# Performance work log

Measured on AMD Instinct MI355X. Metric: run time of the kernel, lower is better.

## Reference

```python
import jax, jax.numpy as jnp
import numpy as np

N_NODES = 370
N_EEG = 64
HID = 64
L = 8
KS = 2
EMB = 16
KTOP = N_NODES // 10  # 37, as in the torch code


def _gcn_norm_dense(A):
    # A[dst, src] dense adjacency. torch_geometric GCNConv gcn_norm:
    # add self-loop weight 1.0 only for nodes lacking one, then D^-1/2 A D^-1/2.
    d0 = jnp.diagonal(A)
    A = A + jnp.diag(jnp.where(d0 > 0, 0.0, 1.0))
    deg = A.sum(axis=1)  # weighted in-degree at dst (incl. self loops)
    dinv = jnp.where(deg > 0, jax.lax.rsqrt(deg), 0.0)
    return dinv[:, None] * A * dinv[None, :]


def _adaptive_adj(emb_src, emb_tgt):
    # softmax(relu(S T^T)) row-wise, keep top-k per row (softmax vals are all >0)
    adj = jax.nn.softmax(jax.nn.relu(emb_src @ emb_tgt.T), axis=-1)
    vals, idx = jax.lax.top_k(adj, KTOP)
    sp = jnp.zeros_like(adj).at[jnp.arange(adj.shape[0])[:, None], idx].set(vals)
    return _gcn_norm_dense(sp)


def _causal_conv(h, w, b, dilation):
    # h: (BN, H, T), w: (H_out, H_in, K); left-pad by (K-1)*dilation => causal
    pad = (w.shape[-1] - 1) * dilation
    out = jax.lax.conv_general_dilated(
        h, w, window_strides=(1,), padding=[(pad, 0)],
        rhs_dilation=(dilation,), dimension_numbers=("NCH", "OIH", "NCH"))
    return out + b[None, :, None]


def _layernorm(x, g, b, eps=1e-5):
    m = x.mean(-1, keepdims=True)
    v = ((x - m) ** 2).mean(-1, keepdims=True)
    return (x - m) * jax.lax.rsqrt(v + eps) * g + b


def _gelu(x):
    return jax.nn.gelu(x, approximate=False)


def setup_inputs() -> dict:
    key = jax.random.key(0)
    ks = iter(jax.random.split(key, 64))
    B, T, E = 8, 64, 7400

    x = jax.random.normal(next(ks), (B, T, N_NODES, HID), jnp.float32)
    src = jax.random.randint(next(ks), (E,), 0, N_NODES, jnp.int32)
    off = jax.random.randint(next(ks), (E,), 1, N_NODES, jnp.int32)
    edge_index = jnp.stack([src, (src + off) % N_NODES])  # self-loop free
    edge_weight = jax.random.uniform(next(ks), (E,), jnp.float32)

    def rn(shape, scale):
        return jax.random.normal(next(ks), shape, jnp.float32) * scale

    s = 1.0 / np.sqrt(HID)
    inp = {
        "x": x, "edge_index": edge_index, "edge_weight": edge_weight,
        "in_W": rn((HID, HID), s), "in_b": rn((HID,), 0.01),
        "gcnf_W": rn((L, HID, HID), s), "gcnf_b": rn((L, HID), 0.01),
        "emb_src": rn((L, N_NODES, EMB), 1.0),  # torch.randn init
        "emb_tgt": rn((L, N_NODES, EMB), 1.0),
        "gcna_W": rn((L, HID, HID), s), "gcna_b": rn((L, HID), 0.01),
        "filt_W": rn((L, HID, HID, KS), s), "filt_b": rn((L, HID), 0.01),
        "gate_W": rn((L, HID, HID, KS), s), "gate_b": rn((L, HID), 0.01),
        "res_W": rn((L, HID, HID), s), "res_b": rn((L, HID), 0.01),
        "skip_W": rn((L, HID, HID), s), "skip_b": rn((L, HID), 0.01),
        "ln_g": jnp.ones((L, HID), jnp.float32), "ln_b": jnp.zeros((L, HID), jnp.float32),
        "end1_W": rn((HID, HID), s), "end1_b": rn((HID,), 0.01),
        "end2_W": rn((HID, HID), s), "end2_b": rn((HID,), 0.01),
        "eeg1_W": rn((N_NODES * HID, 256), 1.0 / np.sqrt(N_NODES * HID)), "eeg1_b": rn((256,), 0.01),
        "eeg2_W": rn((256, N_EEG), 1.0 / 16.0), "eeg2_b": rn((N_EEG,), 0.01),
    }
    return inp


def reference(x, edge_index, edge_weight, in_W, in_b, gcnf_W, gcnf_b,
              emb_src, emb_tgt, gcna_W, gcna_b, filt_W, filt_b, gate_W, gate_b,
              res_W, res_b, skip_W, skip_b, ln_g, ln_b,
              end1_W, end1_b, end2_W, end2_b, eeg1_W, eeg1_b, eeg2_W, eeg2_b):
    B, T, N, H = x.shape
    x = x @ in_W + in_b  # input_proj

    # Fixed (DTI prior) adjacency: same for every layer, build & normalize once.
    A = jnp.zeros((N, N), x.dtype).at[edge_index[1], edge_index[0]].add(edge_weight)
    A = _gcn_norm_dense(A)

    skip_sum = jnp.zeros_like(x)
    for i in range(L):  # fixed small layer count
        dil = 2 ** (i % 4)
        xf = x.reshape(B * T, N, H)
        h_fixed = jnp.einsum("mn,bnh->bmh", A, xf @ gcnf_W[i]) + gcnf_b[i]
        Aa = _adaptive_adj(emb_src[i], emb_tgt[i])
        h_adapt = jnp.einsum("mn,bnh->bmh", Aa, xf @ gcna_W[i]) + gcna_b[i]
        h = (h_fixed + h_adapt).reshape(B, T, N, H)
        h = h.transpose(0, 2, 3, 1).reshape(B * N, H, T)
        h = jnp.tanh(_causal_conv(h, filt_W[i], filt_b[i], dil)) * \
            jax.nn.sigmoid(_causal_conv(h, gate_W[i], gate_b[i], dil))
        # 1x1 convs over channel dim (dropout is identity in eval)
        skip = (jnp.einsum("oi,nit->not", skip_W[i], h) + skip_b[i][None, :, None])
        res = (jnp.einsum("oi,nit->not", res_W[i], h) + res_b[i][None, :, None])
        skip = skip.reshape(B, N, H, T).transpose(0, 3, 1, 2)
        res = res.reshape(B, N, H, T).transpose(0, 3, 1, 2)
        x = _layernorm(res + x, ln_g[i], ln_b[i])
        skip_sum = skip_sum + skip

    h = _gelu(skip_sum) @ end1_W + end1_b
    h = _gelu(h) @ end2_W + end2_b
    h = h.reshape(B, T, N * H)  # GraphToEEG
    h = _gelu(h @ eeg1_W + eeg1_b) @ eeg2_W + eeg2_b
    return h
```

## Files before the change

kernel.cpp:

```cpp
#include <hip/hip_runtime.h>
#include <hip/hip_bf16.h>
#include <math.h>

typedef __attribute__((ext_vector_type(8))) short bf16x8;
typedef __attribute__((ext_vector_type(4))) float f32x4;
typedef unsigned short u16;
typedef unsigned int u32;
typedef unsigned long long u64;

#define NN 370
#define HH 64
#define LL 8
#define TT 64
#define BTOT 512
#define RR (BTOT*NN)
#define KTOPK 37
#define SPLITK 37

__device__ inline u16 f2bf(float f){
  __hip_bfloat16 h = __float2bfloat16(f);
  return __builtin_bit_cast(u16, h);
}
__device__ inline float bf2f(short s){
  u32 v = ((u32)(u16)s) << 16;
  return __builtin_bit_cast(float, v);
}
__device__ inline float gelu_f(float x){ return 0.5f * x * (1.0f + erff(x * 0.70710678118654752440f)); }

__device__ inline void sts16(char* lds, int row, int kb, int stride, bf16x8 v){
  *reinterpret_cast<bf16x8*>(lds + row*stride + (kb ^ ((row&7)<<4))) = v;
}
__device__ inline bf16x8 lds16(const char* lds, int row, int kb, int stride){
  return *reinterpret_cast<const bf16x8*>(lds + row*stride + (kb ^ ((row&7)<<4)));
}
__device__ inline bf16x8 gldB(const char* Bt, int c, int kb, int stride){
  return *reinterpret_cast<const bf16x8*>(Bt + c*stride + (kb ^ ((c&7)<<4)));
}
__device__ inline void copyB(char* dst, const u16* src, int bytes, int tid, int nthr){
  for(int o = tid*16; o < bytes; o += nthr*16)
    *reinterpret_cast<bf16x8*>(dst + o) =
      *reinterpret_cast<const bf16x8*>(reinterpret_cast<const char*>(src) + o);
}

template<int NT, int KT>
__device__ inline void mma_core(const char* sA, const char* sB, int strideA, int strideB,
                                f32x4* acc, int ln, int mt){
#pragma unroll
  for(int nt=0; nt<NT; ++nt) acc[nt] = f32x4{0.f,0.f,0.f,0.f};
#pragma unroll
  for(int kt=0; kt<KT; ++kt){
    int kb = kt*64 + ((ln>>4)<<4);
    bf16x8 a = lds16(sA, mt*16 + (ln&15), kb, strideA);
#pragma unroll
    for(int nt=0; nt<NT; ++nt){
      bf16x8 b = lds16(sB, nt*16 + (ln&15), kb, strideB);
      acc[nt] = __builtin_amdgcn_mfma_f32_16x16x32_bf16(a, b, acc[nt], 0, 0, 0);
    }
  }
}

__global__ void kzero(float* __restrict__ p, size_t n){
  for(size_t i = (size_t)blockIdx.x*256 + threadIdx.x; i < n; i += (size_t)gridDim.x*256) p[i] = 0.f;
}

__global__ void kbuildA(const int* __restrict__ ei, const float* __restrict__ ew, float* __restrict__ Araw, int E){
  int e = blockIdx.x*256 + threadIdx.x;
  if(e < E){
    int src = ei[e], dst = ei[E + e];
    atomicAdd(&Araw[dst*NN + src], ew[e]);
  }
}

__global__ __launch_bounds__(384) void knormF(float* __restrict__ Araw, float* __restrict__ dinvF){
  int i = threadIdx.x;
  if(i < NN){
    float d0 = Araw[i*NN+i];
    if(d0 == 0.f) Araw[i*NN+i] = 1.f;
    float s = 0.f;
    for(int j=0;j<NN;++j) s += Araw[i*NN+j];
    dinvF[i] = rsqrtf(s);
  }
}

__global__ __launch_bounds__(512) void kadapt(const float* __restrict__ esrc, const float* __restrict__ etgt,
                                              float* __restrict__ ArawA, float* __restrict__ dinvA){
  __shared__ float tgT[16][372];
  __shared__ float red[8];
  __shared__ u64 keys[512];
  __shared__ int diagflag;
  int i = blockIdx.x, l = blockIdx.y, tid = threadIdx.x;
  const float* Et = etgt + (size_t)l*NN*16;
  for(int idx = tid; idx < NN*16; idx += 512)
    tgT[idx & 15][idx >> 4] = Et[idx];
  float sr[16];
  const float* Es = esrc + ((size_t)l*NN + i)*16;
#pragma unroll
  for(int k=0;k<16;k++) sr[k] = Es[k];
  if(tid == 0) diagflag = 0;
  __syncthreads();
  bool act = tid < NN;
  float s = 0.f;
  if(act){
    float d = 0.f;
#pragma unroll
    for(int k=0;k<16;k++) d += sr[k]*tgT[k][tid];
    s = fmaxf(d, 0.f);
  }
  float v = act ? s : -1.f;
#pragma unroll
  for(int o=1;o<64;o<<=1) v = fmaxf(v, __shfl_xor(v,o,64));
  if((tid&63)==0) red[tid>>6] = v;
  __syncthreads();
  float mx = red[0];
#pragma unroll
  for(int q=1;q<8;q++) mx = fmaxf(mx, red[q]);
  __syncthreads();
  float e = act ? expf(s - mx) : 0.f;
  float t = e;
#pragma unroll
  for(int o=1;o<64;o<<=1) t += __shfl_xor(t,o,64);
  if((tid&63)==0) red[tid>>6] = t;
  __syncthreads();
  float sum = 0.f;
#pragma unroll
  for(int q=0;q<8;q++) sum += red[q];
  float p = e / sum;
  u32 fb = __builtin_bit_cast(u32, p);
  keys[tid] = act ? ((((u64)fb)<<32) | (u64)(0xFFFFFFFFu - (u32)tid)) : 0ULL;
  __syncthreads();
  for(int k2=2; k2<=512; k2<<=1){
    for(int j=k2>>1; j>0; j>>=1){
      int ixj = tid ^ j;
      if(ixj > tid){
        u64 a = keys[tid], b = keys[ixj];
        bool dirUp = ((tid & k2) == 0);
        if(dirUp ? (a < b) : (a > b)){ keys[tid] = b; keys[ixj] = a; }
      }
      __syncthreads();
    }
  }
  float myval = 0.f; int myidx = -1;
  if(tid < KTOPK){
    u64 kk = keys[tid];
    myidx = (int)(0xFFFFFFFFu - (u32)kk);
    myval = __builtin_bit_cast(float, (u32)(kk>>32));
    if(myidx == i) diagflag = 1;
  }
  __syncthreads();
  float dsum = (tid < KTOPK) ? myval : 0.f;
  if(tid < 64){
#pragma unroll
    for(int o=1;o<64;o<<=1) dsum += __shfl_xor(dsum,o,64);
    if(tid == 0) dinvA[l*NN + i] = rsqrtf(dsum + (diagflag ? 0.f : 1.f));
  }
  if(tid < KTOPK) ArawA[((size_t)l*NN + i)*NN + myidx] = myval;
  if(tid == 0 && !diagflag) ArawA[((size_t)l*NN + i)*NN + i] = 1.f;
}

__global__ void kacat(const float* __restrict__ Araw, const float* __restrict__ ArawA,
                      const float* __restrict__ dinvF, const float* __restrict__ dinvA,
                      u16* __restrict__ Acat){
  int idx = blockIdx.x*256 + threadIdx.x;
  if(idx >= LL*384*768) return;
  int k = idx % 768; int m = (idx / 768) % 384; int l = idx / (768*384);
  float v = 0.f;
  if(m < NN){
    if(k < 384){
      if(k < NN) v = dinvF[m]*Araw[m*NN+k]*dinvF[k];
    } else {
      int n = k - 384;
      if(n < NN) v = dinvA[l*NN+m]*ArawA[((size_t)l*NN+m)*NN+n]*dinvA[l*NN+n];
    }
  }
  Acat[idx] = f2bf(v);
}

__global__ void kbt_small(const float* __restrict__ inW, const float* __restrict__ e1W, const float* __restrict__ e2W,
                          u16* __restrict__ BtIN, u16* __restrict__ BtE1, u16* __restrict__ BtE2){
  const float* W = blockIdx.x==0 ? inW : (blockIdx.x==1 ? e1W : e2W);
  u16* Bt = blockIdx.x==0 ? BtIN : (blockIdx.x==1 ? BtE1 : BtE2);
  for(int idx = threadIdx.x; idx < 4096; idx += 256){
    int c = idx >> 6, k = idx & 63;
    *(u16*)((char*)Bt + c*128 + ((k*2) ^ ((c&7)<<4))) = f2bf(W[k*64 + c]);
  }
}

__global__ void kbt_layer(const float* __restrict__ gcnfW, const float* __restrict__ gcnaW,
                          const float* __restrict__ filtW, const float* __restrict__ gateW,
                          const float* __restrict__ skipW, const float* __restrict__ resW,
                          u16* __restrict__ BtUV, u16* __restrict__ BtCV, u16* __restrict__ BtSR){
  int l = blockIdx.x, which = blockIdx.y;
  if(which == 0){
    u16* Bt = BtUV + (size_t)l*128*64;
    for(int idx=threadIdx.x; idx<8192; idx+=256){
      int c = idx>>6, k = idx&63;
      float v = (c<64) ? gcnfW[(size_t)l*4096 + k*64 + c] : gcnaW[(size_t)l*4096 + k*64 + (c-64)];
      *(u16*)((char*)Bt + c*128 + ((k*2) ^ ((c&7)<<4))) = f2bf(v);
    }
  } else if(which == 1){
    u16* Bt = BtCV + (size_t)l*128*128;
    for(int idx=threadIdx.x; idx<16384; idx+=256){
      int c = idx>>7, k = idx&127;
      const float* W = (c<64) ? filtW : gateW;
      int o = c & 63, ii = k & 63, tap = (k<64) ? 1 : 0;
      float v = W[(size_t)l*8192 + o*128 + ii*2 + tap];
      *(u16*)((char*)Bt + c*256 + ((k*2) ^ ((c&7)<<4))) = f2bf(v);
    }
  } else {
    u16* Bt = BtSR + (size_t)l*128*64;
    for(int idx=threadIdx.x; idx<8192; idx+=256){
      int c = idx>>6, k = idx&63;
      float v = (c<64) ? skipW[(size_t)l*4096 + c*64 + k] : resW[(size_t)l*4096 + (c-64)*64 + k];
      *(u16*)((char*)Bt + c*128 + ((k*2) ^ ((c&7)<<4))) = f2bf(v);
    }
  }
}

__global__ void ktrans(const float* __restrict__ W, u16* __restrict__ Wt){
  __shared__ float tile[64][65];
  int kb = blockIdx.x*64, cb = blockIdx.y*64;
  for(int idx = threadIdx.x; idx < 4096; idx += 256){
    int kk = idx>>6, cc = idx&63;
    tile[kk][cc] = W[(size_t)(kb+kk)*256 + cb+cc];
  }
  __syncthreads();
  for(int idx = threadIdx.x; idx < 4096; idx += 256){
    int cc = idx>>6, kk = idx&63;
    Wt[(size_t)(cb+cc)*23680 + kb+kk] = f2bf(tile[kk][cc]);
  }
}

__global__ __launch_bounds__(256) void krowmm_in(const float* __restrict__ X, const u16* __restrict__ Bt,
                                                 const float* __restrict__ bias,
                                                 u16* __restrict__ xbf){
  int tid = threadIdx.x;
  int w = tid>>6, ln = tid&63, lr = ln&15, hi = ln>>4;
  int kboff = hi<<4;
  size_t r = (size_t)blockIdx.x*64 + w*16 + lr;
  f32x4 acc[4];
#pragma unroll
  for(int i=0;i<4;i++) acc[i] = f32x4{0.f,0.f,0.f,0.f};
  const char* BI = (const char*)Bt;
#pragma unroll
  for(int kt=0; kt<2; ++kt){
    const float* xr = X + r*64 + kt*32 + hi*8;
    float4 pa = ((const float4*)xr)[0], pb = ((const float4*)xr)[1];
    bf16x8 a;
    a[0]=(short)f2bf(pa.x); a[1]=(short)f2bf(pa.y); a[2]=(short)f2bf(pa.z); a[3]=(short)f2bf(pa.w);
    a[4]=(short)f2bf(pb.x); a[5]=(short)f2bf(pb.y); a[6]=(short)f2bf(pb.z); a[7]=(short)f2bf(pb.w);
#pragma unroll
    for(int nt=0; nt<4; ++nt){
      bf16x8 b = gldB(BI, nt*16 + lr, kt*64 + kboff, 128);
      acc[nt] = __builtin_amdgcn_mfma_f32_16x16x32_bf16(a, b, acc[nt], 0, 0, 0);
    }
  }
  size_t r0 = (size_t)blockIdx.x*64;
#pragma unroll
  for(int nt=0; nt<4; ++nt){
    int c = nt*16 + lr;
    float bv = bias[c];
#pragma unroll
    for(int rr=0;rr<4;++rr){
      int row = w*16 + hi*4 + rr;
      xbf[(r0+row)*64 + c] = f2bf(acc[nt][rr] + bv);
    }
  }
}

__global__ __launch_bounds__(1024) void kgcn(const u16* __restrict__ xbf, const u16* __restrict__ BtUV,
                                             const u16* __restrict__ Acat,
                                             const float* __restrict__ bfb, const float* __restrict__ bab,
                                             u16* __restrict__ t2){
  __shared__ char uvt[2*16384];
  int bt2 = blockIdx.x, tid = threadIdx.x;
  int w = tid>>6, ln = tid&63, lr = ln&15, hi = ln>>4;
  int kboff = hi<<4;
  int q = w>>3, wq = w&7;
  int bt = bt2*2 + q;
  const char* xb = (const char*)(xbf + (size_t)bt*NN*64);
  char* uq = uvt + q*16384;
  f32x4 acc[12];
#pragma unroll
  for(int j=0;j<12;j++) acc[j] = f32x4{0.f,0.f,0.f,0.f};
#pragma unroll
  for(int sp=0; sp<6; ++sp){
    int p = sp/3, third = sp - p*3;
    int nl = third*128 + wq*16 + lr;
    bf16x8 a0, a1;
    if(nl < NN){
      a0 = *reinterpret_cast<const bf16x8*>(xb + (size_t)nl*128 + kboff);
      a1 = *reinterpret_cast<const bf16x8*>(xb + (size_t)nl*128 + 64 + kboff);
    } else {
      bf16x8 z = {0,0,0,0,0,0,0,0}; a0 = z; a1 = z;
    }
    f32x4 uv[4];
#pragma unroll
    for(int nt=0;nt<4;++nt) uv[nt] = f32x4{0.f,0.f,0.f,0.f};
#pragma unroll
    for(int nt=0;nt<4;++nt){
      int c = p*64 + nt*16 + lr;
      bf16x8 b0 = gldB((const char*)BtUV, c, kboff, 128);
      bf16x8 b1 = gldB((const char*)BtUV, c, 64 + kboff, 128);
      uv[nt] = __builtin_amdgcn_mfma_f32_16x16x32_bf16(a0, b0, uv[nt], 0,0,0);
      uv[nt] = __builtin_amdgcn_mfma_f32_16x16x32_bf16(a1, b1, uv[nt], 0,0,0);
    }
    __syncthreads();
    int ndl = wq*16 + hi*4;
#pragma unroll
    for(int nt=0;nt<4;++nt){
      int cl = nt*16 + lr;
      u64 pk = (u64)((u32)f2bf(uv[nt][0]) | ((u32)f2bf(uv[nt][1])<<16))
             | ((u64)((u32)f2bf(uv[nt][2]) | ((u32)f2bf(uv[nt][3])<<16)) << 32);
      *(u64*)(uq + cl*256 + ((ndl*2) ^ ((cl&7)<<4))) = pk;
    }
    __syncthreads();
    const char* abase = (const char*)Acat + p*768 + third*256 + kboff;
#pragma unroll
    for(int kt=0; kt<4; ++kt){
      bf16x8 a_0 = *reinterpret_cast<const bf16x8*>(abase + (size_t)((wq*3+0)*16 + lr)*1536 + kt*64);
      bf16x8 a_1 = *reinterpret_cast<const bf16x8*>(abase + (size_t)((wq*3+1)*16 + lr)*1536 + kt*64);
      bf16x8 a_2 = *reinterpret_cast<const bf16x8*>(abase + (size_t)((wq*3+2)*16 + lr)*1536 + kt*64);
      bf16x8 b0 = lds16(uq, 0*16 + lr, kt*64 + kboff, 256);
      bf16x8 b1 = lds16(uq, 1*16 + lr, kt*64 + kboff, 256);
      bf16x8 b2 = lds16(uq, 2*16 + lr, kt*64 + kboff, 256);
      bf16x8 b3 = lds16(uq, 3*16 + lr, kt*64 + kboff, 256);
      acc[0]  = __builtin_amdgcn_mfma_f32_16x16x32_bf16(a_0, b0, acc[0],  0,0,0);
      acc[1]  = __builtin_amdgcn_mfma_f32_16x16x32_bf16(a_0, b1, acc[1],  0,0,0);
      acc[2]  = __builtin_amdgcn_mfma_f32_16x16x32_bf16(a_0, b2, acc[2],  0,0,0);
      acc[3]  = __builtin_amdgcn_mfma_f32_16x16x32_bf16(a_0, b3, acc[3],  0,0,0);
      acc[4]  = __builtin_amdgcn_mfma_f32_16x16x32_bf16(a_1, b0, acc[4],  0,0,0);
      acc[5]  = __builtin_amdgcn_mfma_f32_16x16x32_bf16(a_1, b1, acc[5],  0,0,0);
      acc[6]  = __builtin_amdgcn_mfma_f32_16x16x32_bf16(a_1, b2, acc[6],  0,0,0);
      acc[7]  = __builtin_amdgcn_mfma_f32_16x16x32_bf16(a_1, b3, acc[7],  0,0,0);
      acc[8]  = __builtin_amdgcn_mfma_f32_16x16x32_bf16(a_2, b0, acc[8],  0,0,0);
      acc[9]  = __builtin_amdgcn_mfma_f32_16x16x32_bf16(a_2, b1, acc[9],  0,0,0);
      acc[10] = __builtin_amdgcn_mfma_f32_16x16x32_bf16(a_2, b2, acc[10], 0,0,0);
      acc[11] = __builtin_amdgcn_mfma_f32_16x16x32_bf16(a_2, b3, acc[11], 0,0,0);
    }
  }
#pragma unroll
  for(int mi=0; mi<3; ++mi){
    int mt = wq*3 + mi;
    int mbase = mt*16 + hi*4;
#pragma unroll
    for(int nt=0; nt<4; ++nt){
      int col = nt*16 + lr;
      float bias = bfb[col] + bab[col];
#pragma unroll
      for(int r=0;r<4;++r){
        int m = mbase + r;
        if(m < NN) t2[((size_t)bt*NN + m)*64 + col] = f2bf(acc[mi*4+nt][r] + bias);
      }
    }
  }
}

__global__ __launch_bounds__(256) void kcsr(const u16* __restrict__ t2, const u16* __restrict__ BtC,
                                            const u16* __restrict__ BtS,
                                            const float* __restrict__ fb, const float* __restrict__ gb,
                                            const float* __restrict__ sb, const float* __restrict__ rb,
                                            const float* __restrict__ lng, const float* __restrict__ lnb,
                                            u16* __restrict__ skip,
                                            u16* __restrict__ xbf, int dil, int first, int douv){
  __shared__ char sA[32768];
  int blk = blockIdx.x, tid = threadIdx.x;
  int w = tid>>6, ln = tid&63, lr = ln&15, hi = ln>>4;
  int kboff = hi<<4;
  int r0 = blk*64;
  int r = r0 + w*16 + lr;
  int t = (r / NN) & (TT-1);
  const char* cur = (const char*)t2 + (size_t)r*128;
  const char* prv = cur - (size_t)dil*NN*128;
  bf16x8 a0 = *reinterpret_cast<const bf16x8*>(cur + kboff);
  bf16x8 a1 = *reinterpret_cast<const bf16x8*>(cur + 64 + kboff);
  bf16x8 a2, a3;
  if(t >= dil){
    a2 = *reinterpret_cast<const bf16x8*>(prv + kboff);
    a3 = *reinterpret_cast<const bf16x8*>(prv + 64 + kboff);
  } else {
    bf16x8 z = {0,0,0,0,0,0,0,0}; a2 = z; a3 = z;
  }
  const char* BC = (const char*)BtC;
  f32x4 acc[8];
#pragma unroll
  for(int i=0;i<8;i++) acc[i] = f32x4{0.f,0.f,0.f,0.f};
  bf16x8 afr[4] = {a0, a1, a2, a3};
#pragma unroll
  for(int kt=0; kt<4; ++kt){
    bf16x8 bfr[8];
#pragma unroll
    for(int nt=0; nt<8; ++nt)
      bfr[nt] = gldB(BC, nt*16 + lr, kt*64 + kboff, 256);
#pragma unroll
    for(int nt=0; nt<8; ++nt)
      acc[nt] = __builtin_amdgcn_mfma_f32_16x16x32_bf16(afr[kt], bfr[nt], acc[nt], 0, 0, 0);
  }
  u16 qv[4][4];
#pragma unroll
  for(int nt=0; nt<4; ++nt){
    int o = nt*16 + lr;
    float fbv = fb[o], gbv = gb[o];
#pragma unroll
    for(int rr=0;rr<4;++rr){
      float fv = acc[nt][rr] + fbv;
      float gv = acc[nt+4][rr] + gbv;
      float ef = __expf(-2.f*fv);
      float th = (1.f - ef) / (1.f + ef);
      float sg = 1.f / (1.f + __expf(-gv));
      qv[nt][rr] = f2bf(th * sg);
    }
  }
#pragma unroll
  for(int nt=0; nt<4; ++nt){
    int col = nt*16 + lr;
#pragma unroll
    for(int rr=0;rr<4;++rr){
      int row = w*16 + hi*4 + rr;
      *(u16*)(sA + row*128 + ((col*2) ^ ((row&7)<<4))) = qv[nt][rr];
    }
  }
  __syncthreads();
  const char* BS = (const char*)BtS;
  f32x4 as[8];
#pragma unroll
  for(int i=0;i<8;i++) as[i] = f32x4{0.f,0.f,0.f,0.f};
#pragma unroll
  for(int kt=0; kt<2; ++kt){
    bf16x8 a = lds16(sA, w*16 + lr, kt*64 + kboff, 128);
    bf16x8 bfr[8];
#pragma unroll
    for(int nt=0; nt<8; ++nt)
      bfr[nt] = gldB(BS, nt*16 + lr, kt*64 + kboff, 128);
#pragma unroll
    for(int nt=0; nt<8; ++nt)
      as[nt] = __builtin_amdgcn_mfma_f32_16x16x32_bf16(a, bfr[nt], as[nt], 0, 0, 0);
  }
  __syncthreads();
#pragma unroll
  for(int nt=0; nt<4; ++nt){
    int c = nt*16 + lr;
#pragma unroll
    for(int rr=0;rr<4;++rr){
      int row = w*16 + hi*4 + rr;
      *(float*)(sA + row*512 + (((c)*4)      ^ ((row&7)<<4))) = as[nt][rr];
      *(float*)(sA + row*512 + (((64+c)*4)   ^ ((row&7)<<4))) = as[4+nt][rr];
    }
  }
  __syncthreads();
  int row = tid >> 2, seg = tid & 3;
  int c0 = seg * 16;
  float sk[16], re[16];
#pragma unroll
  for(int j=0;j<4;++j){
    f32x4 vs = *reinterpret_cast<const f32x4*>(sA + row*512 + (((c0 + j*4)*4)      ^ ((row&7)<<4)));
    f32x4 vr = *reinterpret_cast<const f32x4*>(sA + row*512 + (((64 + c0 + j*4)*4) ^ ((row&7)<<4)));
#pragma unroll
    for(int i=0;i<4;++i){ sk[j*4+i] = vs[i]; re[j*4+i] = vr[i]; }
  }
  size_t gr = (size_t)(r0 + row)*64 + c0;
  bf16x8 xv0 = *reinterpret_cast<const bf16x8*>(xbf + gr);
  bf16x8 xv1 = *reinterpret_cast<const bf16x8*>(xbf + gr + 8);
  float y[16]; float s1 = 0.f, s2 = 0.f;
#pragma unroll
  for(int i=0;i<16;++i){
    float xo = bf2f(i < 8 ? xv0[i] : xv1[i-8]);
    float vv = re[i] + rb[c0+i] + xo;
    y[i] = vv; s1 += vv; s2 += vv*vv;
  }
  s1 += __shfl_xor(s1, 1, 64); s1 += __shfl_xor(s1, 2, 64);
  s2 += __shfl_xor(s2, 1, 64); s2 += __shfl_xor(s2, 2, 64);
  float m = s1 * (1.f/64.f);
  float var = s2 * (1.f/64.f) - m*m;
  float rstd = rsqrtf(var + 1e-5f);
  if(douv){
    bf16x8 o0, o1;
#pragma unroll
    for(int i=0;i<16;++i){
      float xo = (y[i] - m) * rstd * lng[c0+i] + lnb[c0+i];
      if(i < 8) o0[i] = (short)f2bf(xo); else o1[i-8] = (short)f2bf(xo);
    }
    *reinterpret_cast<bf16x8*>(xbf + gr) = o0;
    *reinterpret_cast<bf16x8*>(xbf + gr + 8) = o1;
  }
  bf16x8 so0, so1;
  if(first){
#pragma unroll
    for(int i=0;i<16;++i){
      float sv = sk[i] + sb[c0+i];
      if(i < 8) so0[i] = (short)f2bf(sv); else so1[i-8] = (short)f2bf(sv);
    }
  } else {
    bf16x8 sp0 = *reinterpret_cast<const bf16x8*>(skip + gr);
    bf16x8 sp1 = *reinterpret_cast<const bf16x8*>(skip + gr + 8);
#pragma unroll
    for(int i=0;i<16;++i){
      float old = bf2f(i < 8 ? sp0[i] : sp1[i-8]);
      float sv = old + sk[i] + sb[c0+i];
      if(i < 8) so0[i] = (short)f2bf(sv); else so1[i-8] = (short)f2bf(sv);
    }
  }
  *reinterpret_cast<bf16x8*>(skip + gr) = so0;
  *reinterpret_cast<bf16x8*>(skip + gr + 8) = so1;
}

__global__ __launch_bounds__(256) void kend2(const u16* __restrict__ skip, const u16* __restrict__ Bt1,
                                             const u16* __restrict__ Bt2, const float* __restrict__ b1,
                                             const float* __restrict__ b2, u16* __restrict__ h2){
  __shared__ char sA[8192];
  int tid = threadIdx.x;
  int w = tid>>6, ln = tid&63, lr = ln&15, hi = ln>>4;
  int kboff = hi<<4;
  size_t r = (size_t)blockIdx.x*64 + w*16 + lr;
  const char* B1 = (const char*)Bt1;
  const char* B2 = (const char*)Bt2;
  f32x4 acc[4];
#pragma unroll
  for(int i=0;i<4;i++) acc[i] = f32x4{0.f,0.f,0.f,0.f};
#pragma unroll
  for(int kt=0; kt<2; ++kt){
    bf16x8 a = *reinterpret_cast<const bf16x8*>((const char*)skip + r*128 + kt*64 + kboff);
#pragma unroll
    for(int i=0;i<8;i++) a[i] = (short)f2bf(gelu_f(bf2f(a[i])));
#pragma unroll
    for(int nt=0; nt<4; ++nt){
      bf16x8 b = gldB(B1, nt*16 + lr, kt*64 + kboff, 128);
      acc[nt] = __builtin_amdgcn_mfma_f32_16x16x32_bf16(a, b, acc[nt], 0, 0, 0);
    }
  }
  u16 xq[4][4];
#pragma unroll
  for(int nt=0; nt<4; ++nt){
    int c = nt*16 + lr;
    float bv = b1[c];
#pragma unroll
    for(int rr=0;rr<4;++rr) xq[nt][rr] = f2bf(gelu_f(acc[nt][rr] + bv));
  }
#pragma unroll
  for(int nt=0; nt<4; ++nt){
    int col = nt*16 + lr;
#pragma unroll
    for(int rr=0;rr<4;++rr){
      int row = w*16 + hi*4 + rr;
      *(u16*)(sA + row*128 + ((col*2) ^ ((row&7)<<4))) = xq[nt][rr];
    }
  }
  __syncthreads();
  f32x4 a2[4];
#pragma unroll
  for(int i=0;i<4;i++) a2[i] = f32x4{0.f,0.f,0.f,0.f};
#pragma unroll
  for(int kt=0; kt<2; ++kt){
    bf16x8 a = lds16(sA, w*16 + lr, kt*64 + kboff, 128);
#pragma unroll
    for(int nt=0; nt<4; ++nt){
      bf16x8 b = gldB(B2, nt*16 + lr, kt*64 + kboff, 128);
      a2[nt] = __builtin_amdgcn_mfma_f32_16x16x32_bf16(a, b, a2[nt], 0, 0, 0);
    }
  }
  size_t rbase = (size_t)blockIdx.x*64 + w*16 + hi*4;
#pragma unroll
  for(int nt=0; nt<4; ++nt){
    int c = nt*16 + lr;
    float bv = b2[c];
#pragma unroll
    for(int rr=0;rr<4;++rr) h2[(rbase+rr)*64 + c] = f2bf(a2[nt][rr] + bv);
  }
}

__global__ __launch_bounds__(512) void keeg1(const u16* __restrict__ h2, const u16* __restrict__ WtE,
                                             float* __restrict__ part){
  __shared__ char sA[64*128];
  __shared__ char sB[256*128];
  int rowg = blockIdx.x, sp = blockIdx.y;
  int tid = threadIdx.x, w = tid>>6, ln = tid&63;
  f32x4 acc[8];
#pragma unroll
  for(int i=0;i<8;i++) acc[i] = f32x4{0.f,0.f,0.f,0.f};
  int mt = w & 3, ntb = (w>>2)*8;
  for(int ks=0; ks<20; ++ks){
    int k0 = (sp*20 + ks)*32;
    __syncthreads();
    for(int s = tid; s < 256; s += 512){
      int row = s>>2, kc = s&3;
      bf16x8 v = *reinterpret_cast<const bf16x8*>(h2 + (size_t)(rowg*64+row)*23680 + k0 + kc*8);
      sts16(sA, row, kc*16, 128, v);
    }
    for(int s = tid; s < 1024; s += 512){
      int row = s>>2, kc = s&3;
      bf16x8 v = *reinterpret_cast<const bf16x8*>(WtE + (size_t)row*23680 + k0 + kc*8);
      sts16(sB, row, kc*16, 128, v);
    }
    __syncthreads();
    bf16x8 a = lds16(sA, mt*16 + (ln&15), ((ln>>4)<<4), 128);
#pragma unroll
    for(int j=0;j<8;++j){
      bf16x8 b = lds16(sB, (ntb+j)*16 + (ln&15), ((ln>>4)<<4), 128);
      acc[j] = __builtin_amdgcn_mfma_f32_16x16x32_bf16(a, b, acc[j], 0, 0, 0);
    }
  }
  float* dst = part + ((size_t)sp*512 + rowg*64)*256;
#pragma unroll
  for(int j=0;j<8;++j){
    int c = (ntb+j)*16 + (ln&15);
#pragma unroll
    for(int r=0;r<4;++r){
      int row = mt*16 + ((ln>>4)<<2) + r;
      dst[(size_t)row*256 + c] = acc[j][r];
    }
  }
}

__global__ __launch_bounds__(256) void keeg2(const float* __restrict__ part, const float* __restrict__ b1,
                                             const float* __restrict__ W2, const float* __restrict__ b2,
                                             float* __restrict__ out){
  __shared__ float u[256];
  __shared__ float pr[4][64];
  int bt = blockIdx.x, tid = threadIdx.x;
  float sacc = 0.f;
  for(int sp2=0; sp2<SPLITK; ++sp2) sacc += part[((size_t)sp2*512 + bt)*256 + tid];
  u[tid] = gelu_f(sacc + b1[tid]);
  __syncthreads();
  int w = tid>>6, ln = tid&63;
  float acc = 0.f;
  for(int c = w*64; c < (w+1)*64; ++c) acc += u[c] * W2[c*64 + ln];
  pr[w][ln] = acc;
  __syncthreads();
  if(tid < 64)
    out[(size_t)bt*64 + tid] = pr[0][tid]+pr[1][tid]+pr[2][tid]+pr[3][tid] + b2[tid];
}

extern "C" void kernel_launch(void* const* d_in, const int* in_sizes, int n_in,
                              void* d_out, int out_size, void* d_ws, size_t ws_size,
                              hipStream_t stream){
  const float* x_in  = (const float*)d_in[0];
  const int*   ei    = (const int*)d_in[1];
  const float* ew    = (const float*)d_in[2];
  const float* in_W  = (const float*)d_in[3];
  const float* in_b  = (const float*)d_in[4];
  const float* gcnfW = (const float*)d_in[5];
  const float* gcnfb = (const float*)d_in[6];
  const float* esrc  = (const float*)d_in[7];
  const float* etgt  = (const float*)d_in[8];
  const float* gcnaW = (const float*)d_in[9];
  const float* gcnab = (const float*)d_in[10];
  const float* filtW = (const float*)d_in[11];
  const float* filtb = (const float*)d_in[12];
  const float* gateW = (const float*)d_in[13];
  const float* gateb = (const float*)d_in[14];
  const float* resW  = (const float*)d_in[15];
  const float* resb  = (const float*)d_in[16];
  const float* skipW = (const float*)d_in[17];
  const float* skipb = (const float*)d_in[18];
  const float* lng   = (const float*)d_in[19];
  const float* lnb   = (const float*)d_in[20];
  const float* e1W   = (const float*)d_in[21];
  const float* e1b   = (const float*)d_in[22];
  const float* e2W   = (const float*)d_in[23];
  const float* e2b   = (const float*)d_in[24];
  const float* eg1W  = (const float*)d_in[25];
  const float* eg1b  = (const float*)d_in[26];
  const float* eg2W  = (const float*)d_in[27];
  const float* eg2b  = (const float*)d_in[28];
  int E = in_sizes[2];

  char* p = (char*)d_ws;
  auto carve = [&](size_t bytes)->char*{ char* r = p; p += (bytes + 255) & ~(size_t)255; return r; };
  u16*   xbf   = (u16*)  carve((size_t)RR*64*2);
  u16*   skip  = (u16*)  carve((size_t)RR*64*2);
  u16*   t2    = (u16*)  carve((size_t)RR*64*2);
  u16*   h2    = (u16*)  carve((size_t)RR*64*2);
  float* Araw9 = (float*)carve((size_t)9*NN*NN*4);
  float* Araw  = Araw9;
  float* ArawA = Araw9 + (size_t)NN*NN;
  float* dinvF = (float*)carve(NN*4);
  float* dinvA = (float*)carve(LL*NN*4);
  u16*   Acat  = (u16*)  carve((size_t)LL*384*768*2);
  u16*   BtUV  = (u16*)  carve((size_t)LL*128*64*2);
  u16*   BtCV  = (u16*)  carve((size_t)LL*128*128*2);
  u16*   BtSR  = (u16*)  carve((size_t)LL*128*64*2);
  u16*   BtIN  = (u16*)  carve(64*64*2);
  u16*   BtE1  = (u16*)  carve(64*64*2);
  u16*   BtE2  = (u16*)  carve(64*64*2);
  u16*   WtE   = (u16*)  carve((size_t)256*23680*2);
  float* part  = (float*)carve((size_t)SPLITK*512*256*4);

  kzero<<<1024, 256, 0, stream>>>(Araw9, (size_t)9*NN*NN);
  kbuildA<<<(E+255)/256, 256, 0, stream>>>(ei, ew, Araw, E);
  knormF<<<1, 384, 0, stream>>>(Araw, dinvF);
  kadapt<<<dim3(NN, LL), 512, 0, stream>>>(esrc, etgt, ArawA, dinvA);
  kacat<<<(LL*384*768 + 255)/256, 256, 0, stream>>>(Araw, ArawA, dinvF, dinvA, Acat);
  kbt_small<<<3, 256, 0, stream>>>(in_W, e1W, e2W, BtIN, BtE1, BtE2);
  kbt_layer<<<dim3(LL, 3), 256, 0, stream>>>(gcnfW, gcnaW, filtW, gateW, skipW, resW, BtUV, BtCV, BtSR);
  ktrans<<<dim3(370, 4), 256, 0, stream>>>(eg1W, WtE);

  krowmm_in<<<RR/64, 256, 0, stream>>>(x_in, BtIN, in_b, xbf);

  for(int l=0; l<LL; ++l){
    int dil = 1 << (l & 3);
    kgcn<<<BTOT/2, 1024, 0, stream>>>(xbf, BtUV + (size_t)l*8192, Acat + (size_t)l*384*768,
                                      gcnfb + l*64, gcnab + l*64, t2);
    int douv = (l < LL-1) ? 1 : 0;
    kcsr<<<RR/64, 256, 0, stream>>>(t2, BtCV + (size_t)l*16384, BtSR + (size_t)l*8192,
                                    filtb + l*64, gateb + l*64, skipb + l*64, resb + l*64,
                                    lng + l*64, lnb + l*64, skip, xbf, dil, l==0 ? 1 : 0, douv);
  }

  kend2<<<RR/64, 256, 0, stream>>>(skip, BtE1, BtE2, e1b, e2b, h2);
  keeg1<<<dim3(8, SPLITK), 512, 0, stream>>>(h2, WtE, part);
  keeg2<<<BTOT, 256, 0, stream>>>(part, eg1b, eg2W, eg2b, (float*)d_out);
}
```

Baseline: 1.019 ms.

## Double-buffer UV tiles in GCN kernel, one timestep per 512-thread block

The GCN kernel now processes one batch-time slice per 512-thread block instead of two slices per 1024-thread block, and reuses the freed shared memory as a double buffer for the UV tile. The next UV projection is computed while the adjacency MFMA for the current tile runs, which removes one of the two barriers per stage and overlaps the global loads with compute. In exchange it holds more registers for the prefetched UV values, which may lower occupancy, and it launches twice as many blocks.

```diff
diff --git a/kernel.cpp b/kernel.cpp
--- a/kernel.cpp
+++ b/kernel.cpp
@@ -267,25 +267,23 @@
   }
 }
 
-__global__ __launch_bounds__(1024) void kgcn(const u16* __restrict__ xbf, const u16* __restrict__ BtUV,
-                                             const u16* __restrict__ Acat,
-                                             const float* __restrict__ bfb, const float* __restrict__ bab,
-                                             u16* __restrict__ t2){
+__global__ __launch_bounds__(512) void kgcn(const u16* __restrict__ xbf, const u16* __restrict__ BtUV,
+                                            const u16* __restrict__ Acat,
+                                            const float* __restrict__ bfb, const float* __restrict__ bab,
+                                            u16* __restrict__ t2){
   __shared__ char uvt[2*16384];
-  int bt2 = blockIdx.x, tid = threadIdx.x;
+  int bt = blockIdx.x, tid = threadIdx.x;
   int w = tid>>6, ln = tid&63, lr = ln&15, hi = ln>>4;
   int kboff = hi<<4;
-  int q = w>>3, wq = w&7;
-  int bt = bt2*2 + q;
   const char* xb = (const char*)(xbf + (size_t)bt*NN*64);
-  char* uq = uvt + q*16384;
+  const char* BU = (const char*)BtUV;
   f32x4 acc[12];
 #pragma unroll
   for(int j=0;j<12;j++) acc[j] = f32x4{0.f,0.f,0.f,0.f};
-#pragma unroll
-  for(int sp=0; sp<6; ++sp){
+
+  auto UVC = [&](int sp, f32x4* uv){
     int p = sp/3, third = sp - p*3;
-    int nl = third*128 + wq*16 + lr;
+    int nl = third*128 + w*16 + lr;
     bf16x8 a0, a1;
     if(nl < NN){
       a0 = *reinterpret_cast<const bf16x8*>(xb + (size_t)nl*128 + kboff);
@@ -293,19 +291,24 @@
     } else {
       bf16x8 z = {0,0,0,0,0,0,0,0}; a0 = z; a1 = z;
     }
-    f32x4 uv[4];
 #pragma unroll
     for(int nt=0;nt<4;++nt) uv[nt] = f32x4{0.f,0.f,0.f,0.f};
 #pragma unroll
     for(int nt=0;nt<4;++nt){
       int c = p*64 + nt*16 + lr;
-      bf16x8 b0 = gldB((const char*)BtUV, c, kboff, 128);
-      bf16x8 b1 = gldB((const char*)BtUV, c, 64 + kboff, 128);
+      bf16x8 b0 = gldB(BU, c, kboff, 128);
+      bf16x8 b1 = gldB(BU, c, 64 + kboff, 128);
       uv[nt] = __builtin_amdgcn_mfma_f32_16x16x32_bf16(a0, b0, uv[nt], 0,0,0);
       uv[nt] = __builtin_amdgcn_mfma_f32_16x16x32_bf16(a1, b1, uv[nt], 0,0,0);
     }
-    __syncthreads();
-    int ndl = wq*16 + hi*4;
+  };
+
+  f32x4 uv[4];
+  UVC(0, uv);
+#pragma unroll
+  for(int sp=0; sp<6; ++sp){
+    char* uq = uvt + (sp&1)*16384;
+    int ndl = w*16 + hi*4;
 #pragma unroll
     for(int nt=0;nt<4;++nt){
       int cl = nt*16 + lr;
@@ -314,12 +317,15 @@
       *(u64*)(uq + cl*256 + ((ndl*2) ^ ((cl&7)<<4))) = pk;
     }
     __syncthreads();
+    f32x4 uvn[4];
+    if(sp < 5) UVC(sp+1, uvn);
+    int p = sp/3, third = sp - p*3;
     const char* abase = (const char*)Acat + p*768 + third*256 + kboff;
 #pragma unroll
     for(int kt=0; kt<4; ++kt){
-      bf16x8 a_0 = *reinterpret_cast<const bf16x8*>(abase + (size_t)((wq*3+0)*16 + lr)*1536 + kt*64);
-      bf16x8 a_1 = *reinterpret_cast<const bf16x8*>(abase + (size_t)((wq*3+1)*16 + lr)*1536 + kt*64);
-      bf16x8 a_2 = *reinterpret_cast<const bf16x8*>(abase + (size_t)((wq*3+2)*16 + lr)*1536 + kt*64);
+      bf16x8 a_0 = *reinterpret_cast<const bf16x8*>(abase + (size_t)((w*3+0)*16 + lr)*1536 + kt*64);
+      bf16x8 a_1 = *reinterpret_cast<const bf16x8*>(abase + (size_t)((w*3+1)*16 + lr)*1536 + kt*64);
+      bf16x8 a_2 = *reinterpret_cast<const bf16x8*>(abase + (size_t)((w*3+2)*16 + lr)*1536 + kt*64);
       bf16x8 b0 = lds16(uq, 0*16 + lr, kt*64 + kboff, 256);
       bf16x8 b1 = lds16(uq, 1*16 + lr, kt*64 + kboff, 256);
       bf16x8 b2 = lds16(uq, 2*16 + lr, kt*64 + kboff, 256);
@@ -337,10 +343,14 @@
       acc[10] = __builtin_amdgcn_mfma_f32_16x16x32_bf16(a_2, b2, acc[10], 0,0,0);
       acc[11] = __builtin_amdgcn_mfma_f32_16x16x32_bf16(a_2, b3, acc[11], 0,0,0);
     }
+    if(sp < 5){
+#pragma unroll
+      for(int nt=0;nt<4;++nt) uv[nt] = uvn[nt];
+    }
   }
 #pragma unroll
   for(int mi=0; mi<3; ++mi){
-    int mt = wq*3 + mi;
+    int mt = w*3 + mi;
     int mbase = mt*16 + hi*4;
 #pragma unroll
     for(int nt=0; nt<4; ++nt){
@@ -697,8 +707,8 @@
 
   for(int l=0; l<LL; ++l){
     int dil = 1 << (l & 3);
-    kgcn<<<BTOT/2, 1024, 0, stream>>>(xbf, BtUV + (size_t)l*8192, Acat + (size_t)l*384*768,
-                                      gcnfb + l*64, gcnab + l*64, t2);
+    kgcn<<<BTOT, 512, 0, stream>>>(xbf, BtUV + (size_t)l*8192, Acat + (size_t)l*384*768,
+                                   gcnfb + l*64, gcnab + l*64, t2);
     int douv = (l < LL-1) ? 1 : 0;
     kcsr<<<RR/64, 256, 0, stream>>>(t2, BtCV + (size_t)l*16384, BtSR + (size_t)l*8192,
                                     filtb + l*64, gateb + l*64, skipb + l*64, resb + l*64,
```

After: 1.040 ms. 2.0% more time.

## Fuse GCN feature projection into producer kernels and write transposed intermediate

Applied to the files above, without the earlier changes.

Moves the per-layer x@[Wf|Wa] projection out of kgcn and into the kernel that produces x: krowmm_in for layer 0 and kcsr's layernorm epilogue for later layers. The result is stored to global memory in a node-transposed, zero-padded layout (t1T). kgcn then streams both operands straight from global memory, with no LDS staging and no __syncthreads, one batch-time slice per 512-thread block. This removes the in-kernel projection and its barriers, at the cost of an extra 49KB-per-slice intermediate round-trip through HBM and an added zero-padding kernel. knormF is also parallelized to one wave per row.

```diff
diff --git a/kernel.cpp b/kernel.cpp
--- a/kernel.cpp
+++ b/kernel.cpp
@@ -16,6 +16,7 @@
 #define RR (BTOT*NN)
 #define KTOPK 37
 #define SPLITK 37
+#define T1TSTRIDE 49152
 
 __device__ inline u16 f2bf(float f){
   __hip_bfloat16 h = __float2bfloat16(f);
@@ -36,31 +37,44 @@
 __device__ inline bf16x8 gldB(const char* Bt, int c, int kb, int stride){
   return *reinterpret_cast<const bf16x8*>(Bt + c*stride + (kb ^ ((c&7)<<4)));
 }
-__device__ inline void copyB(char* dst, const u16* src, int bytes, int tid, int nthr){
-  for(int o = tid*16; o < bytes; o += nthr*16)
-    *reinterpret_cast<bf16x8*>(dst + o) =
-      *reinterpret_cast<const bf16x8*>(reinterpret_cast<const char*>(src) + o);
-}
-
-template<int NT, int KT>
-__device__ inline void mma_core(const char* sA, const char* sB, int strideA, int strideB,
-                                f32x4* acc, int ln, int mt){
-#pragma unroll
-  for(int nt=0; nt<NT; ++nt) acc[nt] = f32x4{0.f,0.f,0.f,0.f};
-#pragma unroll
-  for(int kt=0; kt<KT; ++kt){
-    int kb = kt*64 + ((ln>>4)<<4);
-    bf16x8 a = lds16(sA, mt*16 + (ln&15), kb, strideA);
-#pragma unroll
-    for(int nt=0; nt<NT; ++nt){
-      bf16x8 b = lds16(sB, nt*16 + (ln&15), kb, strideB);
-      acc[nt] = __builtin_amdgcn_mfma_f32_16x16x32_bf16(a, b, acc[nt], 0, 0, 0);
+
+__device__ inline void uv_write(u16* __restrict__ t1T, const f32x4* a2, int rbase, int lr){
+  int bt0 = rbase / NN;
+  int nd0 = rbase - bt0*NN;
+  if(nd0 + 3 < NN){
+    u16* dst = t1T + (size_t)bt0*T1TSTRIDE + nd0;
+#pragma unroll
+    for(int nt=0; nt<8; ++nt){
+      int c = nt*16 + lr;
+      u64 pk = (u64)((u32)f2bf(a2[nt][0]) | ((u32)f2bf(a2[nt][1])<<16))
+             | ((u64)((u32)f2bf(a2[nt][2]) | ((u32)f2bf(a2[nt][3])<<16)) << 32);
+      *(u64*)(dst + (size_t)c*384) = pk;
+    }
+  } else {
+#pragma unroll
+    for(int r=0;r<4;++r){
+      int rg = rbase + r;
+      int btr = rg / NN, ndr = rg - btr*NN;
+#pragma unroll
+      for(int nt=0; nt<8; ++nt){
+        int c = nt*16 + lr;
+        t1T[(size_t)btr*T1TSTRIDE + (size_t)c*384 + ndr] = f2bf(a2[nt][r]);
+      }
     }
   }
 }
 
 __global__ void kzero(float* __restrict__ p, size_t n){
   for(size_t i = (size_t)blockIdx.x*256 + threadIdx.x; i < n; i += (size_t)gridDim.x*256) p[i] = 0.f;
+}
+
+__global__ void kzpad(u16* __restrict__ t1T){
+  int idx = blockIdx.x*256 + threadIdx.x;
+  if(idx < BTOT*128){
+    u16* d = t1T + (size_t)idx*384 + NN;
+#pragma unroll
+    for(int i=0;i<14;i++) d[i] = 0;
+  }
 }
 
 __global__ void kbuildA(const int* __restrict__ ei, const float* __restrict__ ew, float* __restrict__ Araw, int E){
@@ -71,13 +85,15 @@
   }
 }
 
-__global__ __launch_bounds__(384) void knormF(float* __restrict__ Araw, float* __restrict__ dinvF){
-  int i = threadIdx.x;
-  if(i < NN){
-    float d0 = Araw[i*NN+i];
-    if(d0 == 0.f) Araw[i*NN+i] = 1.f;
-    float s = 0.f;
-    for(int j=0;j<NN;++j) s += Araw[i*NN+j];
+__global__ __launch_bounds__(64) void knormF(float* __restrict__ Araw, float* __restrict__ dinvF){
+  int i = blockIdx.x, ln = threadIdx.x;
+  float d0 = Araw[i*NN + i];
+  float s = 0.f;
+  for(int j = ln; j < NN; j += 64) s += Araw[i*NN + j];
+#pragma unroll
+  for(int o=1;o<64;o<<=1) s += __shfl_xor(s, o, 64);
+  if(ln == 0){
+    if(d0 == 0.f){ Araw[i*NN+i] = 1.f; s += 1.f; }
     dinvF[i] = rsqrtf(s);
   }
 }
@@ -231,8 +247,10 @@
 }
 
 __global__ __launch_bounds__(256) void krowmm_in(const float* __restrict__ X, const u16* __restrict__ Bt,
+                                                 const u16* __restrict__ BtUV0,
                                                  const float* __restrict__ bias,
-                                                 u16* __restrict__ xbf){
+                                                 u16* __restrict__ xbf, u16* __restrict__ t1T){
+  __shared__ char sA[8192];
   int tid = threadIdx.x;
   int w = tid>>6, ln = tid&63, lr = ln&15, hi = ln>>4;
   int kboff = hi<<4;
@@ -262,68 +280,57 @@
 #pragma unroll
     for(int rr=0;rr<4;++rr){
       int row = w*16 + hi*4 + rr;
-      xbf[(r0+row)*64 + c] = f2bf(acc[nt][rr] + bv);
-    }
-  }
-}
-
-__global__ __launch_bounds__(1024) void kgcn(const u16* __restrict__ xbf, const u16* __restrict__ BtUV,
-                                             const u16* __restrict__ Acat,
-                                             const float* __restrict__ bfb, const float* __restrict__ bab,
-                                             u16* __restrict__ t2){
-  __shared__ char uvt[2*16384];
-  int bt2 = blockIdx.x, tid = threadIdx.x;
+      u16 q = f2bf(acc[nt][rr] + bv);
+      xbf[(r0+row)*64 + c] = q;
+      *(u16*)(sA + row*128 + ((c*2) ^ ((row&7)<<4))) = q;
+    }
+  }
+  __syncthreads();
+  f32x4 a2[8];
+#pragma unroll
+  for(int i=0;i<8;i++) a2[i] = f32x4{0.f,0.f,0.f,0.f};
+  const char* BU = (const char*)BtUV0;
+#pragma unroll
+  for(int kt=0; kt<2; ++kt){
+    bf16x8 a = lds16(sA, w*16 + lr, kt*64 + kboff, 128);
+#pragma unroll
+    for(int nt=0; nt<8; ++nt){
+      bf16x8 b = gldB(BU, nt*16 + lr, kt*64 + kboff, 128);
+      a2[nt] = __builtin_amdgcn_mfma_f32_16x16x32_bf16(a, b, a2[nt], 0, 0, 0);
+    }
+  }
+  uv_write(t1T, a2, (int)r0 + w*16 + hi*4, lr);
+}
+
+__global__ __launch_bounds__(512) void kgcn(const u16* __restrict__ t1T, const u16* __restrict__ Acat,
+                                            const float* __restrict__ bfb, const float* __restrict__ bab,
+                                            u16* __restrict__ t2){
+  int bt = blockIdx.x, tid = threadIdx.x;
   int w = tid>>6, ln = tid&63, lr = ln&15, hi = ln>>4;
   int kboff = hi<<4;
-  int q = w>>3, wq = w&7;
-  int bt = bt2*2 + q;
-  const char* xb = (const char*)(xbf + (size_t)bt*NN*64);
-  char* uq = uvt + q*16384;
+  const char* tb = (const char*)(t1T + (size_t)bt*T1TSTRIDE);
   f32x4 acc[12];
 #pragma unroll
   for(int j=0;j<12;j++) acc[j] = f32x4{0.f,0.f,0.f,0.f};
-#pragma unroll
-  for(int sp=0; sp<6; ++sp){
-    int p = sp/3, third = sp - p*3;
-    int nl = third*128 + wq*16 + lr;
-    bf16x8 a0, a1;
-    if(nl < NN){
-      a0 = *reinterpret_cast<const bf16x8*>(xb + (size_t)nl*128 + kboff);
-      a1 = *reinterpret_cast<const bf16x8*>(xb + (size_t)nl*128 + 64 + kboff);
-    } else {
-      bf16x8 z = {0,0,0,0,0,0,0,0}; a0 = z; a1 = z;
-    }
-    f32x4 uv[4];
-#pragma unroll
-    for(int nt=0;nt<4;++nt) uv[nt] = f32x4{0.f,0.f,0.f,0.f};
-#pragma unroll
-    for(int nt=0;nt<4;++nt){
-      int c = p*64 + nt*16 + lr;
-      bf16x8 b0 = gldB((const char*)BtUV, c, kboff, 128);
-      bf16x8 b1 = gldB((const char*)BtUV, c, 64 + kboff, 128);
-      uv[nt] = __builtin_amdgcn_mfma_f32_16x16x32_bf16(a0, b0, uv[nt], 0,0,0);
-      uv[nt] = __builtin_amdgcn_mfma_f32_16x16x32_bf16(a1, b1, uv[nt], 0,0,0);
-    }
-    __syncthreads();
-    int ndl = wq*16 + hi*4;
-#pragma unroll
-    for(int nt=0;nt<4;++nt){
-      int cl = nt*16 + lr;
-      u64 pk = (u64)((u32)f2bf(uv[nt][0]) | ((u32)f2bf(uv[nt][1])<<16))
-             | ((u64)((u32)f2bf(uv[nt][2]) | ((u32)f2bf(uv[nt][3])<<16)) << 32);
-      *(u64*)(uq + cl*256 + ((ndl*2) ^ ((cl&7)<<4))) = pk;
-    }
-    __syncthreads();
-    const char* abase = (const char*)Acat + p*768 + third*256 + kboff;
-#pragma unroll
-    for(int kt=0; kt<4; ++kt){
-      bf16x8 a_0 = *reinterpret_cast<const bf16x8*>(abase + (size_t)((wq*3+0)*16 + lr)*1536 + kt*64);
-      bf16x8 a_1 = *reinterpret_cast<const bf16x8*>(abase + (size_t)((wq*3+1)*16 + lr)*1536 + kt*64);
-      bf16x8 a_2 = *reinterpret_cast<const bf16x8*>(abase + (size_t)((wq*3+2)*16 + lr)*1536 + kt*64);
-      bf16x8 b0 = lds16(uq, 0*16 + lr, kt*64 + kboff, 256);
-      bf16x8 b1 = lds16(uq, 1*16 + lr, kt*64 + kboff, 256);
-      bf16x8 b2 = lds16(uq, 2*16 + lr, kt*64 + kboff, 256);
-      bf16x8 b3 = lds16(uq, 3*16 + lr, kt*64 + kboff, 256);
+  const char* ar0 = (const char*)Acat + (size_t)((w*3+0)*16 + lr)*1536 + kboff;
+  const char* ar1 = (const char*)Acat + (size_t)((w*3+1)*16 + lr)*1536 + kboff;
+  const char* ar2 = (const char*)Acat + (size_t)((w*3+2)*16 + lr)*1536 + kboff;
+  const char* br0 = tb + (size_t)(0*16 + lr)*768 + kboff;
+  const char* br1 = tb + (size_t)(1*16 + lr)*768 + kboff;
+  const char* br2 = tb + (size_t)(2*16 + lr)*768 + kboff;
+  const char* br3 = tb + (size_t)(3*16 + lr)*768 + kboff;
+#pragma unroll
+  for(int p=0; p<2; ++p){
+    int ao = p*768, bo = p*64*768;
+#pragma unroll
+    for(int kt=0; kt<12; ++kt){
+      bf16x8 a_0 = *reinterpret_cast<const bf16x8*>(ar0 + ao + kt*64);
+      bf16x8 a_1 = *reinterpret_cast<const bf16x8*>(ar1 + ao + kt*64);
+      bf16x8 a_2 = *reinterpret_cast<const bf16x8*>(ar2 + ao + kt*64);
+      bf16x8 b0 = *reinterpret_cast<const bf16x8*>(br0 + bo + kt*64);
+      bf16x8 b1 = *reinterpret_cast<const bf16x8*>(br1 + bo + kt*64);
+      bf16x8 b2 = *reinterpret_cast<const bf16x8*>(br2 + bo + kt*64);
+      bf16x8 b3 = *reinterpret_cast<const bf16x8*>(br3 + bo + kt*64);
       acc[0]  = __builtin_amdgcn_mfma_f32_16x16x32_bf16(a_0, b0, acc[0],  0,0,0);
       acc[1]  = __builtin_amdgcn_mfma_f32_16x16x32_bf16(a_0, b1, acc[1],  0,0,0);
       acc[2]  = __builtin_amdgcn_mfma_f32_16x16x32_bf16(a_0, b2, acc[2],  0,0,0);
@@ -340,7 +347,7 @@
   }
 #pragma unroll
   for(int mi=0; mi<3; ++mi){
-    int mt = wq*3 + mi;
+    int mt = w*3 + mi;
     int mbase = mt*16 + hi*4;
 #pragma unroll
     for(int nt=0; nt<4; ++nt){
@@ -356,12 +363,12 @@
 }
 
 __global__ __launch_bounds__(256) void kcsr(const u16* __restrict__ t2, const u16* __restrict__ BtC,
-                                            const u16* __restrict__ BtS,
+                                            const u16* __restrict__ BtS, const u16* __restrict__ BtUVn,
                                             const float* __restrict__ fb, const float* __restrict__ gb,
                                             const float* __restrict__ sb, const float* __restrict__ rb,
                                             const float* __restrict__ lng, const float* __restrict__ lnb,
-                                            u16* __restrict__ skip,
-                                            u16* __restrict__ xbf, int dil, int first, int douv){
+                                            u16* __restrict__ skip, u16* __restrict__ xbf,
+                                            u16* __restrict__ t1T, int dil, int first, int douv){
   __shared__ char sA[32768];
   int blk = blockIdx.x, tid = threadIdx.x;
   int w = tid>>6, ln = tid&63, lr = ln&15, hi = ln>>4;
@@ -373,18 +380,18 @@
   const char* prv = cur - (size_t)dil*NN*128;
   bf16x8 a0 = *reinterpret_cast<const bf16x8*>(cur + kboff);
   bf16x8 a1 = *reinterpret_cast<const bf16x8*>(cur + 64 + kboff);
-  bf16x8 a2, a3;
+  bf16x8 a2f, a3f;
   if(t >= dil){
-    a2 = *reinterpret_cast<const bf16x8*>(prv + kboff);
-    a3 = *reinterpret_cast<const bf16x8*>(prv + 64 + kboff);
+    a2f = *reinterpret_cast<const bf16x8*>(prv + kboff);
+    a3f = *reinterpret_cast<const bf16x8*>(prv + 64 + kboff);
   } else {
-    bf16x8 z = {0,0,0,0,0,0,0,0}; a2 = z; a3 = z;
+    bf16x8 z = {0,0,0,0,0,0,0,0}; a2f = z; a3f = z;
   }
   const char* BC = (const char*)BtC;
   f32x4 acc[8];
 #pragma unroll
   for(int i=0;i<8;i++) acc[i] = f32x4{0.f,0.f,0.f,0.f};
-  bf16x8 afr[4] = {a0, a1, a2, a3};
+  bf16x8 afr[4] = {a0, a1, a2f, a3f};
 #pragma unroll
   for(int kt=0; kt<4; ++kt){
     bf16x8 bfr[8];
@@ -472,8 +479,8 @@
   float m = s1 * (1.f/64.f);
   float var = s2 * (1.f/64.f) - m*m;
   float rstd = rsqrtf(var + 1e-5f);
+  bf16x8 o0, o1;
   if(douv){
-    bf16x8 o0, o1;
 #pragma unroll
     for(int i=0;i<16;++i){
       float xo = (y[i] - m) * rstd * lng[c0+i] + lnb[c0+i];
@@ -501,6 +508,25 @@
   }
   *reinterpret_cast<bf16x8*>(skip + gr) = so0;
   *reinterpret_cast<bf16x8*>(skip + gr + 8) = so1;
+  if(!douv) return;
+  __syncthreads();
+  *reinterpret_cast<bf16x8*>(sA + row*128 + ((c0*2)       ^ ((row&7)<<4))) = o0;
+  *reinterpret_cast<bf16x8*>(sA + row*128 + (((c0+8)*2)   ^ ((row&7)<<4))) = o1;
+  __syncthreads();
+  const char* BU = (const char*)BtUVn;
+  f32x4 a2[8];
+#pragma unroll
+  for(int i=0;i<8;i++) a2[i] = f32x4{0.f,0.f,0.f,0.f};
+#pragma unroll
+  for(int kt=0; kt<2; ++kt){
+    bf16x8 a = lds16(sA, w*16 + lr, kt*64 + kboff, 128);
+#pragma unroll
+    for(int nt=0; nt<8; ++nt){
+      bf16x8 b = gldB(BU, nt*16 + lr, kt*64 + kboff, 128);
+      a2[nt] = __builtin_amdgcn_mfma_f32_16x16x32_bf16(a, b, a2[nt], 0, 0, 0);
+    }
+  }
+  uv_write(t1T, a2, r0 + w*16 + hi*4, lr);
 }
 
 __global__ __launch_bounds__(256) void kend2(const u16* __restrict__ skip, const u16* __restrict__ Bt1,
@@ -669,6 +695,7 @@
   u16*   skip  = (u16*)  carve((size_t)RR*64*2);
   u16*   t2    = (u16*)  carve((size_t)RR*64*2);
   u16*   h2    = (u16*)  carve((size_t)RR*64*2);
+  u16*   t1T   = (u16*)  carve((size_t)BTOT*T1TSTRIDE*2);
   float* Araw9 = (float*)carve((size_t)9*NN*NN*4);
   float* Araw  = Araw9;
   float* ArawA = Araw9 + (size_t)NN*NN;
@@ -685,24 +712,26 @@
   float* part  = (float*)carve((size_t)SPLITK*512*256*4);
 
   kzero<<<1024, 256, 0, stream>>>(Araw9, (size_t)9*NN*NN);
+  kzpad<<<(BTOT*128 + 255)/256, 256, 0, stream>>>(t1T);
   kbuildA<<<(E+255)/256, 256, 0, stream>>>(ei, ew, Araw, E);
-  knormF<<<1, 384, 0, stream>>>(Araw, dinvF);
+  knormF<<<NN, 64, 0, stream>>>(Araw, dinvF);
   kadapt<<<dim3(NN, LL), 512, 0, stream>>>(esrc, etgt, ArawA, dinvA);
   kacat<<<(LL*384*768 + 255)/256, 256, 0, stream>>>(Araw, ArawA, dinvF, dinvA, Acat);
   kbt_small<<<3, 256, 0, stream>>>(in_W, e1W, e2W, BtIN, BtE1, BtE2);
   kbt_layer<<<dim3(LL, 3), 256, 0, stream>>>(gcnfW, gcnaW, filtW, gateW, skipW, resW, BtUV, BtCV, BtSR);
   ktrans<<<dim3(370, 4), 256, 0, stream>>>(eg1W, WtE);
 
-  krowmm_in<<<RR/64, 256, 0, stream>>>(x_in, BtIN, in_b, xbf);
+  krowmm_in<<<RR/64, 256, 0, stream>>>(x_in, BtIN, BtUV, in_b, xbf, t1T);
 
   for(int l=0; l<LL; ++l){
     int dil = 1 << (l & 3);
-    kgcn<<<BTOT/2, 1024, 0, stream>>>(xbf, BtUV + (size_t)l*8192, Acat + (size_t)l*384*768,
-                                      gcnfb + l*64, gcnab + l*64, t2);
+    kgcn<<<BTOT, 512, 0, stream>>>(t1T, Acat + (size_t)l*384*768,
+                                   gcnfb + l*64, gcnab + l*64, t2);
     int douv = (l < LL-1) ? 1 : 0;
     kcsr<<<RR/64, 256, 0, stream>>>(t2, BtCV + (size_t)l*16384, BtSR + (size_t)l*8192,
+                                    BtUV + (size_t)((l+1)&7)*8192,
                                     filtb + l*64, gateb + l*64, skipb + l*64, resb + l*64,
-                                    lng + l*64, lnb + l*64, skip, xbf, dil, l==0 ? 1 : 0, douv);
+                                    lng + l*64, lnb + l*64, skip, xbf, t1T, dil, l==0 ? 1 : 0, douv);
   }
 
   kend2<<<RR/64, 256, 0, stream>>>(skip, BtE1, BtE2, e1b, e2b, h2);
```

Measured after the change: 1.371 ms. 34.5% more time.
